# Performance work log

Measured on AMD Instinct MI355X. Metric: run time of the kernel, lower is better.

## Reference

```python
import jax, jax.numpy as jnp
import numpy as np

N_NODES = 50000
N_EDGES = 800000
FEAT_DIM = 16
HIDDEN = 128
N_LAYERS = 4
OUT_DIM = 12
N_GRAPHS = 1024

def setup_inputs() -> dict:
    key = jax.random.key(0)
    ks = jax.random.split(key, 8)
    return {
        "x": jax.random.normal(ks[0], (N_NODES, FEAT_DIM), jnp.float32),
        "edge_index": jax.random.randint(ks[1], (2, N_EDGES), 0, N_NODES, dtype=jnp.int32),
        "edge_attr": jnp.zeros((N_EDGES, 4), jnp.float32),
        "batch_idx": jnp.sort(jax.random.randint(ks[2], (N_NODES,), 0, N_GRAPHS, dtype=jnp.int32)),
        # node-embed MLP: Linear(16,128) -> relu -> Linear(128,128)
        "W_e1": jax.random.normal(ks[3], (FEAT_DIM, HIDDEN), jnp.float32) * 0.1,
        "b_e1": jnp.zeros((HIDDEN,), jnp.float32),
        "W_e2": jax.random.normal(ks[4], (HIDDEN, HIDDEN), jnp.float32) * 0.05,
        "b_e2": jnp.zeros((HIDDEN,), jnp.float32),
        # stacked GCNConv weights/biases for 4 layers
        "W_g": jax.random.normal(ks[5], (N_LAYERS, HIDDEN, HIDDEN), jnp.float32) * 0.05,
        "b_g": jnp.zeros((N_LAYERS, HIDDEN), jnp.float32),
        # output Linear(128,12)
        "W_o": jax.random.normal(ks[6], (HIDDEN, OUT_DIM), jnp.float32) * 0.05,
        "b_o": jnp.zeros((OUT_DIM,), jnp.float32),
    }

def _gcn_layer(h_in, src, dst, W, b):
    # PyG GCNConv with add_self_loops=True, symmetric normalization:
    # out_i = sum_{j in N(i) u {i}} (d_i d_j)^{-1/2} (x_j W) + b
    h = h_in @ W                                   # [N, H]
    deg = jnp.zeros((N_NODES,), h.dtype).at[dst].add(1.0) + 1.0  # +1 self-loop
    dinv = jax.lax.rsqrt(deg)                      # [N]
    norm = dinv[src] * dinv[dst]                   # [E]
    msg = h[src] * norm[:, None]                   # gather + scale  [E, H]
    agg = jnp.zeros_like(h).at[dst].add(msg)       # scatter-add to targets
    agg = agg + h * (dinv * dinv)[:, None]         # self-loop term
    return agg + b

def reference(x, edge_index, edge_attr, batch_idx, W_e1, b_e1, W_e2, b_e2, W_g, b_g, W_o, b_o):
    del edge_attr  # use_edge_attribution=False; GCNConv ignores edge features
    src, dst = edge_index[0], edge_index[1]
    # node embedding MLP
    h = jax.nn.relu(x @ W_e1 + b_e1) @ W_e2 + b_e2
    for i in range(N_LAYERS):
        h = jax.nn.relu(_gcn_layer(h, src, dst, W_g[i], b_g[i]))
        # dropout is identity in eval mode
    # scatter-mean pooling over graphs
    sums = jax.ops.segment_sum(h, batch_idx, num_segments=N_GRAPHS)
    cnts = jax.ops.segment_sum(jnp.ones((N_NODES,), h.dtype), batch_idx, num_segments=N_GRAPHS)
    pooled = sums / jnp.maximum(cnts, 1.0)[:, None]
    return pooled @ W_o + b_o
```

## Files before the change

### kernel.cpp

```cpp
#include <hip/hip_runtime.h>

#define N_NODES 50000
#define N_EDGES 800000
#define FEAT    16
#define HID     128
#define NLAYERS 4
#define OUTD    12
#define NGRAPH  1024
#define SCAN_NB 196

__device__ inline float4 f4zero() { return make_float4(0.f, 0.f, 0.f, 0.f); }
__device__ inline float4 f4fma(float a, float4 w, float4 acc) {
    acc.x = fmaf(a, w.x, acc.x);
    acc.y = fmaf(a, w.y, acc.y);
    acc.z = fmaf(a, w.z, acc.z);
    acc.w = fmaf(a, w.w, acc.w);
    return acc;
}
__device__ inline float4 f4add(float4 a, float4 b) {
    return make_float4(a.x + b.x, a.y + b.y, a.z + b.z, a.w + b.w);
}

__global__ void k_deg(const int* __restrict__ ei, int* __restrict__ degi) {
    int e = blockIdx.x * 256 + threadIdx.x;
    if (e < N_EDGES) atomicAdd(&degi[ei[N_EDGES + e]], 1);
}

__global__ void k_dinv(const int* __restrict__ degi, float* __restrict__ dinv) {
    int i = blockIdx.x * 256 + threadIdx.x;
    if (i < N_NODES) dinv[i] = rsqrtf((float)degi[i] + 1.0f);
}

__global__ void k_scan_part(const int* __restrict__ degi, int* __restrict__ part) {
    __shared__ int s[256];
    int t = threadIdx.x;
    int i = blockIdx.x * 256 + t;
    int v = (i < N_NODES) ? degi[i] : 0;
    s[t] = v;
    __syncthreads();
    for (int st = 128; st > 0; st >>= 1) {
        if (t < st) s[t] += s[t + st];
        __syncthreads();
    }
    if (t == 0) part[blockIdx.x] = s[0];
}

__global__ void k_scan_mid(int* __restrict__ part) {
    __shared__ int s[256];
    int t = threadIdx.x;
    int v = (t < SCAN_NB) ? part[t] : 0;
    s[t] = v;
    __syncthreads();
    for (int st = 1; st < 256; st <<= 1) {
        int u = (t >= st) ? s[t - st] : 0;
        __syncthreads();
        s[t] += u;
        __syncthreads();
    }
    if (t < SCAN_NB) part[t] = s[t] - v;
}

__global__ void k_scan_final(const int* __restrict__ degi, const int* __restrict__ part,
                             int* __restrict__ offs) {
    __shared__ int s[256];
    int t = threadIdx.x;
    int i = blockIdx.x * 256 + t;
    int v = (i < N_NODES) ? degi[i] : 0;
    s[t] = v;
    __syncthreads();
    for (int st = 1; st < 256; st <<= 1) {
        int u = (t >= st) ? s[t - st] : 0;
        __syncthreads();
        s[t] += u;
        __syncthreads();
    }
    if (i <= N_NODES) offs[i] = s[t] - v + part[blockIdx.x];
}

__global__ void k_fill(const int* __restrict__ ei, const int* __restrict__ offs,
                       const float* __restrict__ dinv,
                       int* __restrict__ cursor, int* __restrict__ csr,
                       float* __restrict__ csrnm) {
    int e = blockIdx.x * 256 + threadIdx.x;
    if (e < N_EDGES) {
        int srcv = ei[e];
        int dstv = ei[N_EDGES + e];
        int p = atomicAdd(&cursor[dstv], 1);
        int slot = offs[dstv] + p;
        csr[slot]   = srcv;
        csrnm[slot] = dinv[srcv];
    }
}

#define EM 32
__global__ void __launch_bounds__(256) k_embed1(
        const float* __restrict__ x,
        const float* __restrict__ W1, const float* __restrict__ b1,
        float* __restrict__ t_out) {
    __shared__ float x_l[EM][FEAT];
    int t = threadIdx.x;
    long n0 = (long)blockIdx.x * EM;
    if (t < 128) {
        int r  = t >> 2;
        int c4 = (t & 3) << 2;
        long n = n0 + r;
        float4 v = (n < N_NODES) ? *(const float4*)&x[n * FEAT + c4] : f4zero();
        *(float4*)&x_l[r][c4] = v;
    }
    __syncthreads();
    int fgrp = t & 31, ngrp = t >> 5;
    int f4 = fgrp << 2;
    float4 acc0 = f4zero(), acc1 = f4zero(), acc2 = f4zero(), acc3 = f4zero();
#pragma unroll
    for (int k = 0; k < FEAT; ++k) {
        float4 w = *(const float4*)&W1[k * HID + f4];
        acc0 = f4fma(x_l[ngrp * 4 + 0][k], w, acc0);
        acc1 = f4fma(x_l[ngrp * 4 + 1][k], w, acc1);
        acc2 = f4fma(x_l[ngrp * 4 + 2][k], w, acc2);
        acc3 = f4fma(x_l[ngrp * 4 + 3][k], w, acc3);
    }
    float4 bv = *(const float4*)&b1[f4];
    acc0 = f4add(acc0, bv); acc1 = f4add(acc1, bv);
    acc2 = f4add(acc2, bv); acc3 = f4add(acc3, bv);
    acc0.x = fmaxf(acc0.x, 0.f); acc0.y = fmaxf(acc0.y, 0.f); acc0.z = fmaxf(acc0.z, 0.f); acc0.w = fmaxf(acc0.w, 0.f);
    acc1.x = fmaxf(acc1.x, 0.f); acc1.y = fmaxf(acc1.y, 0.f); acc1.z = fmaxf(acc1.z, 0.f); acc1.w = fmaxf(acc1.w, 0.f);
    acc2.x = fmaxf(acc2.x, 0.f); acc2.y = fmaxf(acc2.y, 0.f); acc2.z = fmaxf(acc2.z, 0.f); acc2.w = fmaxf(acc2.w, 0.f);
    acc3.x = fmaxf(acc3.x, 0.f); acc3.y = fmaxf(acc3.y, 0.f); acc3.z = fmaxf(acc3.z, 0.f); acc3.w = fmaxf(acc3.w, 0.f);
    long n;
    n = n0 + ngrp * 4 + 0; if (n < N_NODES) *(float4*)&t_out[n * HID + f4] = acc0;
    n = n0 + ngrp * 4 + 1; if (n < N_NODES) *(float4*)&t_out[n * HID + f4] = acc1;
    n = n0 + ngrp * 4 + 2; if (n < N_NODES) *(float4*)&t_out[n * HID + f4] = acc2;
    n = n0 + ngrp * 4 + 3; if (n < N_NODES) *(float4*)&t_out[n * HID + f4] = acc3;
}

#define GM 64
__global__ void __launch_bounds__(256) k_gemm(
        const float* __restrict__ A, const float* __restrict__ W,
        const float* __restrict__ bias, float* __restrict__ B) {
    __shared__ float a_l[GM][HID];
    int t = threadIdx.x;
    long n0 = (long)blockIdx.x * GM;
#pragma unroll
    for (int i = 0; i < 8; ++i) {
        int p  = t + 256 * i;
        int r  = p >> 5;
        int c4 = (p & 31) << 2;
        long n = n0 + r;
        float4 v = (n < N_NODES) ? *(const float4*)&A[n * HID + c4] : f4zero();
        *(float4*)&a_l[r][c4] = v;
    }
    __syncthreads();
    int fgrp = t & 31, ngrp = t >> 5;
    int f4 = fgrp << 2;
    float4 acc[8];
#pragma unroll
    for (int r = 0; r < 8; ++r) acc[r] = f4zero();
#pragma unroll 8
    for (int k = 0; k < HID; ++k) {
        float4 w = *(const float4*)&W[k * HID + f4];
#pragma unroll
        for (int r = 0; r < 8; ++r)
            acc[r] = f4fma(a_l[ngrp * 8 + r][k], w, acc[r]);
    }
    if (bias) {
        float4 bv = *(const float4*)&bias[f4];
#pragma unroll
        for (int r = 0; r < 8; ++r) acc[r] = f4add(acc[r], bv);
    }
#pragma unroll
    for (int r = 0; r < 8; ++r) {
        long n = n0 + ngrp * 8 + r;
        if (n < N_NODES) *(float4*)&B[n * HID + f4] = acc[r];
    }
}

__global__ void __launch_bounds__(256) k_agg(
        const float* __restrict__ hp,
        const int* __restrict__ csr, const float* __restrict__ csrnm,
        const int* __restrict__ offs,
        const float* __restrict__ dinv, const float* __restrict__ bias,
        float* __restrict__ hout) {
    int t = threadIdx.x;
    int lane = t & 63;
    int w = t >> 6;
    int i = blockIdx.x * 4 + w;
    if (i >= N_NODES) return;
    float di = dinv[i];
    int s0 = offs[i], s1 = offs[i + 1];
    const float2* hp2 = (const float2*)hp;
    float2 self = hp2[(long)i * 64 + lane];
    float2 bv = ((const float2*)bias)[lane];
    float ax = fmaf(di * di, self.x, bv.x);
    float ay = fmaf(di * di, self.y, bv.y);
    for (int base = s0; base < s1; base += 64) {
        int n = s1 - base; if (n > 64) n = 64;
        int last = n - 1;
        int idx = base + lane;
        int   sv_l = (lane < n) ? csr[idx]        : 0;
        float nm_l = (lane < n) ? csrnm[idx] * di : 0.f;
        for (int k = 0; k < n; k += 8) {
            int a[8]; float m[8];
#pragma unroll
            for (int u = 0; u < 8; ++u) {
                int kk = k + u;
                int ks = kk < last ? kk : last;
                a[u] = __shfl(sv_l, ks);
                float mu = __shfl(nm_l, ks);
                m[u] = (kk < n) ? mu : 0.f;
            }
            float2 v[8];
#pragma unroll
            for (int u = 0; u < 8; ++u) v[u] = hp2[(long)a[u] * 64 + lane];
#pragma unroll
            for (int u = 0; u < 8; ++u) {
                ax = fmaf(m[u], v[u].x, ax);
                ay = fmaf(m[u], v[u].y, ay);
            }
        }
    }
    float2 r;
    r.x = fmaxf(ax, 0.f);
    r.y = fmaxf(ay, 0.f);
    ((float2*)hout)[(long)i * 64 + lane] = r;
}

#define PN 16
__global__ void __launch_bounds__(256) k_pool(
        const float* __restrict__ h, const int* __restrict__ batch,
        float* __restrict__ pooled, float* __restrict__ cnt) {
    int t = threadIdx.x;
    int lane = t & 31, grp = t >> 5;
    long n0 = ((long)blockIdx.x * 8 + grp) * PN;
    if (n0 >= N_NODES) return;
    long n1 = n0 + PN; if (n1 > N_NODES) n1 = N_NODES;
    const float4* h4 = (const float4*)h;
    float4 run = f4zero();
    int curg = batch[n0];
    int c = 0;
    for (long n = n0; n < n1; ++n) {
        int g = batch[n];
        if (g != curg) {
            float* pb = &pooled[(long)curg * HID + (lane << 2)];
            atomicAdd(pb + 0, run.x); atomicAdd(pb + 1, run.y);
            atomicAdd(pb + 2, run.z); atomicAdd(pb + 3, run.w);
            if (lane == 0) atomicAdd(&cnt[curg], (float)c);
            run = f4zero(); c = 0; curg = g;
        }
        run = f4add(run, h4[n * 32 + lane]);
        ++c;
    }
    float* pb = &pooled[(long)curg * HID + (lane << 2)];
    atomicAdd(pb + 0, run.x); atomicAdd(pb + 1, run.y);
    atomicAdd(pb + 2, run.z); atomicAdd(pb + 3, run.w);
    if (lane == 0) atomicAdd(&cnt[curg], (float)c);
}

__global__ void __launch_bounds__(HID) k_out(
        const float* __restrict__ pooled, const float* __restrict__ cnt,
        const float* __restrict__ Wo, const float* __restrict__ bo,
        float* __restrict__ out) {
    __shared__ float p[HID];
    int g = blockIdx.x;
    int f = threadIdx.x;
    float inv = 1.0f / fmaxf(cnt[g], 1.0f);
    p[f] = pooled[g * HID + f] * inv;
    __syncthreads();
    if (f < OUTD) {
        float acc = bo[f];
#pragma unroll 8
        for (int k = 0; k < HID; ++k) acc += p[k] * Wo[k * OUTD + f];
        out[g * OUTD + f] = acc;
    }
}

extern "C" void kernel_launch(void* const* d_in, const int* in_sizes, int n_in,
                              void* d_out, int out_size, void* d_ws, size_t ws_size,
                              hipStream_t stream) {
    const float* x    = (const float*)d_in[0];
    const int*   ei   = (const int*)d_in[1];
    const int*   bidx = (const int*)d_in[3];
    const float* We1  = (const float*)d_in[4];
    const float* be1  = (const float*)d_in[5];
    const float* We2  = (const float*)d_in[6];
    const float* be2  = (const float*)d_in[7];
    const float* Wg   = (const float*)d_in[8];
    const float* bg   = (const float*)d_in[9];
    const float* Wo   = (const float*)d_in[10];
    const float* bo   = (const float*)d_in[11];
    float* out = (float*)d_out;

    char* ws = (char*)d_ws;
    size_t o = 0;
    auto take = [&](size_t bytes) { size_t r = o; o += (bytes + 255) & ~(size_t)255; return r; };
    size_t off_degi   = take((size_t)N_NODES * 4);
    size_t off_cursor = take((size_t)N_NODES * 4);
    size_t off_pooled = take((size_t)NGRAPH * HID * 4);
    size_t off_cnt    = take((size_t)NGRAPH * 4);
    size_t zero_bytes = o;
    size_t off_dinv   = take((size_t)N_NODES * 4);
    size_t off_offs   = take((size_t)(N_NODES + 1) * 4);
    size_t off_part   = take((size_t)256 * 4);
    size_t off_csr    = take((size_t)N_EDGES * 4);
    size_t off_csrnm  = take((size_t)N_EDGES * 4);
    size_t off_hA     = take((size_t)N_NODES * HID * 4);
    size_t off_hB     = take((size_t)N_NODES * HID * 4);

    int*   degi   = (int*)(ws + off_degi);
    int*   cursor = (int*)(ws + off_cursor);
    float* pooled = (float*)(ws + off_pooled);
    float* cnt    = (float*)(ws + off_cnt);
    float* dinv   = (float*)(ws + off_dinv);
    int*   offs   = (int*)(ws + off_offs);
    int*   part   = (int*)(ws + off_part);
    int*   csr    = (int*)(ws + off_csr);
    float* csrnm  = (float*)(ws + off_csrnm);
    float* hA     = (float*)(ws + off_hA);
    float* hB     = (float*)(ws + off_hB);

    hipMemsetAsync(d_ws, 0, zero_bytes, stream);

    k_deg<<<(N_EDGES + 255) / 256, 256, 0, stream>>>(ei, degi);
    k_dinv<<<(N_NODES + 255) / 256, 256, 0, stream>>>(degi, dinv);
    k_scan_part<<<SCAN_NB, 256, 0, stream>>>(degi, part);
    k_scan_mid<<<1, 256, 0, stream>>>(part);
    k_scan_final<<<SCAN_NB, 256, 0, stream>>>(degi, part, offs);
    k_fill<<<(N_EDGES + 255) / 256, 256, 0, stream>>>(ei, offs, dinv, cursor, csr, csrnm);

    k_embed1<<<(N_NODES + EM - 1) / EM, 256, 0, stream>>>(x, We1, be1, hB);
    int gemm_grid = (N_NODES + GM - 1) / GM;
    k_gemm<<<gemm_grid, 256, 0, stream>>>(hB, We2, be2, hA);

    for (int l = 0; l < NLAYERS; ++l) {
        k_gemm<<<gemm_grid, 256, 0, stream>>>(hA, Wg + (size_t)l * HID * HID, nullptr, hB);
        k_agg<<<(N_NODES + 3) / 4, 256, 0, stream>>>(hB, csr, csrnm, offs, dinv,
                                                     bg + (size_t)l * HID, hA);
    }

    k_pool<<<(N_NODES + 8 * PN - 1) / (8 * PN), 256, 0, stream>>>(hA, bidx, pooled, cnt);
    k_out<<<NGRAPH, HID, 0, stream>>>(pooled, cnt, Wo, bo, out);
}
```

Baseline: 594.4 us.

## Fuse embedding MLP, pack edge records, vectorize GEMM k-loop, widen agg unroll

Merges the two embedding linear layers into one kernel that keeps the hidden activations in shared memory, so the intermediate round trip through global memory goes away. Source index and normalization are packed into one int2 edge record, so the aggregation does a single load per edge. The GEMM inner loop now reads float4 from shared memory with a k-step of 4, and the aggregation gather unroll grows from 8 to 16 to keep more loads in flight. The cost is more register pressure in the agg and GEMM kernels, plus a larger shared-memory footprint in the fused embed kernel.

```diff
diff --git a/kernel.cpp b/kernel.cpp
--- a/kernel.cpp
+++ b/kernel.cpp
@@ -20,6 +20,9 @@
 __device__ inline float4 f4add(float4 a, float4 b) {
     return make_float4(a.x + b.x, a.y + b.y, a.z + b.z, a.w + b.w);
 }
+__device__ inline float4 f4relu(float4 a) {
+    return make_float4(fmaxf(a.x, 0.f), fmaxf(a.y, 0.f), fmaxf(a.z, 0.f), fmaxf(a.w, 0.f));
+}
 
 __global__ void k_deg(const int* __restrict__ ei, int* __restrict__ degi) {
     int e = blockIdx.x * 256 + threadIdx.x;
@@ -79,28 +82,27 @@
 
 __global__ void k_fill(const int* __restrict__ ei, const int* __restrict__ offs,
                        const float* __restrict__ dinv,
-                       int* __restrict__ cursor, int* __restrict__ csr,
-                       float* __restrict__ csrnm) {
+                       int* __restrict__ cursor, int2* __restrict__ erec) {
     int e = blockIdx.x * 256 + threadIdx.x;
     if (e < N_EDGES) {
         int srcv = ei[e];
         int dstv = ei[N_EDGES + e];
         int p = atomicAdd(&cursor[dstv], 1);
-        int slot = offs[dstv] + p;
-        csr[slot]   = srcv;
-        csrnm[slot] = dinv[srcv];
-    }
-}
-
-#define EM 32
-__global__ void __launch_bounds__(256) k_embed1(
+        erec[offs[dstv] + p] = make_int2(srcv, __float_as_int(dinv[srcv]));
+    }
+}
+
+#define GM 64
+__global__ void __launch_bounds__(256) k_embed_fused(
         const float* __restrict__ x,
         const float* __restrict__ W1, const float* __restrict__ b1,
-        float* __restrict__ t_out) {
-    __shared__ float x_l[EM][FEAT];
-    int t = threadIdx.x;
-    long n0 = (long)blockIdx.x * EM;
-    if (t < 128) {
+        const float* __restrict__ W2, const float* __restrict__ b2,
+        float* __restrict__ outp) {
+    __shared__ float x_l[GM][FEAT];
+    __shared__ float a_l[GM][HID];
+    int t = threadIdx.x;
+    long n0 = (long)blockIdx.x * GM;
+    {
         int r  = t >> 2;
         int c4 = (t & 3) << 2;
         long n = n0 + r;
@@ -110,33 +112,66 @@
     __syncthreads();
     int fgrp = t & 31, ngrp = t >> 5;
     int f4 = fgrp << 2;
-    float4 acc0 = f4zero(), acc1 = f4zero(), acc2 = f4zero(), acc3 = f4zero();
-#pragma unroll
-    for (int k = 0; k < FEAT; ++k) {
-        float4 w = *(const float4*)&W1[k * HID + f4];
-        acc0 = f4fma(x_l[ngrp * 4 + 0][k], w, acc0);
-        acc1 = f4fma(x_l[ngrp * 4 + 1][k], w, acc1);
-        acc2 = f4fma(x_l[ngrp * 4 + 2][k], w, acc2);
-        acc3 = f4fma(x_l[ngrp * 4 + 3][k], w, acc3);
-    }
-    float4 bv = *(const float4*)&b1[f4];
-    acc0 = f4add(acc0, bv); acc1 = f4add(acc1, bv);
-    acc2 = f4add(acc2, bv); acc3 = f4add(acc3, bv);
-    acc0.x = fmaxf(acc0.x, 0.f); acc0.y = fmaxf(acc0.y, 0.f); acc0.z = fmaxf(acc0.z, 0.f); acc0.w = fmaxf(acc0.w, 0.f);
-    acc1.x = fmaxf(acc1.x, 0.f); acc1.y = fmaxf(acc1.y, 0.f); acc1.z = fmaxf(acc1.z, 0.f); acc1.w = fmaxf(acc1.w, 0.f);
-    acc2.x = fmaxf(acc2.x, 0.f); acc2.y = fmaxf(acc2.y, 0.f); acc2.z = fmaxf(acc2.z, 0.f); acc2.w = fmaxf(acc2.w, 0.f);
-    acc3.x = fmaxf(acc3.x, 0.f); acc3.y = fmaxf(acc3.y, 0.f); acc3.z = fmaxf(acc3.z, 0.f); acc3.w = fmaxf(acc3.w, 0.f);
-    long n;
-    n = n0 + ngrp * 4 + 0; if (n < N_NODES) *(float4*)&t_out[n * HID + f4] = acc0;
-    n = n0 + ngrp * 4 + 1; if (n < N_NODES) *(float4*)&t_out[n * HID + f4] = acc1;
-    n = n0 + ngrp * 4 + 2; if (n < N_NODES) *(float4*)&t_out[n * HID + f4] = acc2;
-    n = n0 + ngrp * 4 + 3; if (n < N_NODES) *(float4*)&t_out[n * HID + f4] = acc3;
-}
-
-#define GM 64
+    {
+        float4 acc[8];
+#pragma unroll
+        for (int r = 0; r < 8; ++r) acc[r] = f4zero();
+#pragma unroll
+        for (int k4 = 0; k4 < 4; ++k4) {
+            float4 wv[4];
+#pragma unroll
+            for (int kk = 0; kk < 4; ++kk)
+                wv[kk] = *(const float4*)&W1[(k4 * 4 + kk) * HID + f4];
+            float4 xv[8];
+#pragma unroll
+            for (int r = 0; r < 8; ++r)
+                xv[r] = *(const float4*)&x_l[ngrp * 8 + r][k4 << 2];
+#pragma unroll
+            for (int r = 0; r < 8; ++r) {
+                acc[r] = f4fma(xv[r].x, wv[0], acc[r]);
+                acc[r] = f4fma(xv[r].y, wv[1], acc[r]);
+                acc[r] = f4fma(xv[r].z, wv[2], acc[r]);
+                acc[r] = f4fma(xv[r].w, wv[3], acc[r]);
+            }
+        }
+        float4 bv = *(const float4*)&b1[f4];
+#pragma unroll
+        for (int r = 0; r < 8; ++r)
+            *(float4*)&a_l[ngrp * 8 + r][f4] = f4relu(f4add(acc[r], bv));
+    }
+    __syncthreads();
+    float4 acc[8];
+#pragma unroll
+    for (int r = 0; r < 8; ++r) acc[r] = f4zero();
+#pragma unroll 4
+    for (int k4 = 0; k4 < 32; ++k4) {
+        float4 wv[4];
+#pragma unroll
+        for (int kk = 0; kk < 4; ++kk)
+            wv[kk] = *(const float4*)&W2[(k4 * 4 + kk) * HID + f4];
+        float4 av[8];
+#pragma unroll
+        for (int r = 0; r < 8; ++r)
+            av[r] = *(const float4*)&a_l[ngrp * 8 + r][k4 << 2];
+#pragma unroll
+        for (int r = 0; r < 8; ++r) {
+            acc[r] = f4fma(av[r].x, wv[0], acc[r]);
+            acc[r] = f4fma(av[r].y, wv[1], acc[r]);
+            acc[r] = f4fma(av[r].z, wv[2], acc[r]);
+            acc[r] = f4fma(av[r].w, wv[3], acc[r]);
+        }
+    }
+    float4 bv = *(const float4*)&b2[f4];
+#pragma unroll
+    for (int r = 0; r < 8; ++r) {
+        long n = n0 + ngrp * 8 + r;
+        if (n < N_NODES) *(float4*)&outp[n * HID + f4] = f4add(acc[r], bv);
+    }
+}
+
 __global__ void __launch_bounds__(256) k_gemm(
         const float* __restrict__ A, const float* __restrict__ W,
-        const float* __restrict__ bias, float* __restrict__ B) {
+        float* __restrict__ B) {
     __shared__ float a_l[GM][HID];
     int t = threadIdx.x;
     long n0 = (long)blockIdx.x * GM;
@@ -155,17 +190,23 @@
     float4 acc[8];
 #pragma unroll
     for (int r = 0; r < 8; ++r) acc[r] = f4zero();
-#pragma unroll 8
-    for (int k = 0; k < HID; ++k) {
-        float4 w = *(const float4*)&W[k * HID + f4];
+#pragma unroll 4
+    for (int k4 = 0; k4 < 32; ++k4) {
+        float4 wv[4];
+#pragma unroll
+        for (int kk = 0; kk < 4; ++kk)
+            wv[kk] = *(const float4*)&W[(k4 * 4 + kk) * HID + f4];
+        float4 av[8];
 #pragma unroll
         for (int r = 0; r < 8; ++r)
-            acc[r] = f4fma(a_l[ngrp * 8 + r][k], w, acc[r]);
-    }
-    if (bias) {
-        float4 bv = *(const float4*)&bias[f4];
-#pragma unroll
-        for (int r = 0; r < 8; ++r) acc[r] = f4add(acc[r], bv);
+            av[r] = *(const float4*)&a_l[ngrp * 8 + r][k4 << 2];
+#pragma unroll
+        for (int r = 0; r < 8; ++r) {
+            acc[r] = f4fma(av[r].x, wv[0], acc[r]);
+            acc[r] = f4fma(av[r].y, wv[1], acc[r]);
+            acc[r] = f4fma(av[r].z, wv[2], acc[r]);
+            acc[r] = f4fma(av[r].w, wv[3], acc[r]);
+        }
     }
 #pragma unroll
     for (int r = 0; r < 8; ++r) {
@@ -176,8 +217,7 @@
 
 __global__ void __launch_bounds__(256) k_agg(
         const float* __restrict__ hp,
-        const int* __restrict__ csr, const float* __restrict__ csrnm,
-        const int* __restrict__ offs,
+        const int2* __restrict__ erec, const int* __restrict__ offs,
         const float* __restrict__ dinv, const float* __restrict__ bias,
         float* __restrict__ hout) {
     int t = threadIdx.x;
@@ -195,24 +235,24 @@
     for (int base = s0; base < s1; base += 64) {
         int n = s1 - base; if (n > 64) n = 64;
         int last = n - 1;
-        int idx = base + lane;
-        int   sv_l = (lane < n) ? csr[idx]        : 0;
-        float nm_l = (lane < n) ? csrnm[idx] * di : 0.f;
-        for (int k = 0; k < n; k += 8) {
-            int a[8]; float m[8];
-#pragma unroll
-            for (int u = 0; u < 8; ++u) {
+        int2 e = (lane < n) ? erec[base + lane] : make_int2(0, 0);
+        int   sv_l = e.x;
+        float nm_l = __int_as_float(e.y);
+        for (int k = 0; k < n; k += 16) {
+            int a[16]; float m[16];
+#pragma unroll
+            for (int u = 0; u < 16; ++u) {
                 int kk = k + u;
                 int ks = kk < last ? kk : last;
                 a[u] = __shfl(sv_l, ks);
                 float mu = __shfl(nm_l, ks);
-                m[u] = (kk < n) ? mu : 0.f;
+                m[u] = (kk < n) ? mu * di : 0.f;
             }
-            float2 v[8];
-#pragma unroll
-            for (int u = 0; u < 8; ++u) v[u] = hp2[(long)a[u] * 64 + lane];
-#pragma unroll
-            for (int u = 0; u < 8; ++u) {
+            float2 v[16];
+#pragma unroll
+            for (int u = 0; u < 16; ++u) v[u] = hp2[(long)a[u] * 64 + lane];
+#pragma unroll
+            for (int u = 0; u < 16; ++u) {
                 ax = fmaf(m[u], v[u].x, ax);
                 ay = fmaf(m[u], v[u].y, ay);
             }
@@ -300,8 +340,7 @@
     size_t off_dinv   = take((size_t)N_NODES * 4);
     size_t off_offs   = take((size_t)(N_NODES + 1) * 4);
     size_t off_part   = take((size_t)256 * 4);
-    size_t off_csr    = take((size_t)N_EDGES * 4);
-    size_t off_csrnm  = take((size_t)N_EDGES * 4);
+    size_t off_erec   = take((size_t)N_EDGES * 8);
     size_t off_hA     = take((size_t)N_NODES * HID * 4);
     size_t off_hB     = take((size_t)N_NODES * HID * 4);
 
@@ -312,8 +351,7 @@
     float* dinv   = (float*)(ws + off_dinv);
     int*   offs   = (int*)(ws + off_offs);
     int*   part   = (int*)(ws + off_part);
-    int*   csr    = (int*)(ws + off_csr);
-    float* csrnm  = (float*)(ws + off_csrnm);
+    int2*  erec   = (int2*)(ws + off_erec);
     float* hA     = (float*)(ws + off_hA);
     float* hB     = (float*)(ws + off_hB);
 
@@ -324,15 +362,14 @@
     k_scan_part<<<SCAN_NB, 256, 0, stream>>>(degi, part);
     k_scan_mid<<<1, 256, 0, stream>>>(part);
     k_scan_final<<<SCAN_NB, 256, 0, stream>>>(degi, part, offs);
-    k_fill<<<(N_EDGES + 255) / 256, 256, 0, stream>>>(ei, offs, dinv, cursor, csr, csrnm);
-
-    k_embed1<<<(N_NODES + EM - 1) / EM, 256, 0, stream>>>(x, We1, be1, hB);
+    k_fill<<<(N_EDGES + 255) / 256, 256, 0, stream>>>(ei, offs, dinv, cursor, erec);
+
     int gemm_grid = (N_NODES + GM - 1) / GM;
-    k_gemm<<<gemm_grid, 256, 0, stream>>>(hB, We2, be2, hA);
+    k_embed_fused<<<gemm_grid, 256, 0, stream>>>(x, We1, be1, We2, be2, hA);
 
     for (int l = 0; l < NLAYERS; ++l) {
-        k_gemm<<<gemm_grid, 256, 0, stream>>>(hA, Wg + (size_t)l * HID * HID, nullptr, hB);
-        k_agg<<<(N_NODES + 3) / 4, 256, 0, stream>>>(hB, csr, csrnm, offs, dinv,
+        k_gemm<<<gemm_grid, 256, 0, stream>>>(hA, Wg + (size_t)l * HID * HID, hB);
+        k_agg<<<(N_NODES + 3) / 4, 256, 0, stream>>>(hB, erec, offs, dinv,
                                                      bg + (size_t)l * HID, hA);
     }
 
```

Result: no change. 601.9 us (+1.3%).
